# Optimization experiments

Hardware: AMD Instinct MI355X
Metric: run time of the kernel (lower is better)

Reference implementation:

```python
import jax, jax.numpy as jnp
import numpy as np

B, T, H = 128, 1024, 512


def setup_inputs() -> dict:
    key = jax.random.key(0)
    ks = jax.random.split(key, 14)
    s = 1.0 / np.sqrt(H)
    u = lambda k, shape: jax.random.uniform(k, shape, jnp.float32, -s, s)
    return {
        "x": jax.random.normal(ks[0], (B, T, 1), jnp.float32),
        "mask": jax.random.randint(ks[1], (B, T, 1), 0, 2).astype(bool),
        # forward GRU (PyTorch layout: weight_ih [3H,1], weight_hh [3H,H], gate order r,z,n)
        "wf_ih": u(ks[2], (3 * H, 1)),
        "wf_hh": u(ks[3], (3 * H, H)),
        "bf_ih": u(ks[4], (3 * H,)),
        "bf_hh": u(ks[5], (3 * H,)),
        # backward GRU
        "wb_ih": u(ks[6], (3 * H, 1)),
        "wb_hh": u(ks[7], (3 * H, H)),
        "bb_ih": u(ks[8], (3 * H,)),
        "bb_hh": u(ks[9], (3 * H,)),
        # predictor: Linear(H,H) -> ReLU -> Linear(H,1) -> Tanh
        "p_w1": u(ks[10], (H, H)),
        "p_b1": u(ks[11], (H,)),
        "p_w2": u(ks[12], (1, H)),
        "p_b2": u(ks[13], (1,)),
    }


def _gru_cell(h, x_in, w_ih, w_hh, b_ih, b_hh):
    # h: [B,H], x_in: [B,1]; PyTorch GRU gate order (r, z, n)
    gi = x_in @ w_ih.T + b_ih  # [B,3H]
    gh = h @ w_hh.T + b_hh     # [B,3H]
    i_r, i_z, i_n = jnp.split(gi, 3, axis=-1)
    h_r, h_z, h_n = jnp.split(gh, 3, axis=-1)
    r = jax.nn.sigmoid(i_r + h_r)
    z = jax.nn.sigmoid(i_z + h_z)
    n = jnp.tanh(i_n + r * h_n)
    return (1.0 - z) * n + z * h


def reference(x, mask, wf_ih, wf_hh, bf_ih, bf_hh, wb_ih, wb_hh, bb_ih, bb_hh,
              p_w1, p_b1, p_w2, p_b2):
    bsz = x.shape[0]
    hid = wf_hh.shape[1]

    def predictor(h):  # [B,H] -> [B,1]
        return jnp.tanh(jax.nn.relu(h @ p_w1.T + p_b1) @ p_w2.T + p_b2)

    xs_f = jnp.swapaxes(x, 0, 1)      # [T,B,1]
    ms_f = jnp.swapaxes(mask, 0, 1)   # [T,B,1]
    xs_b = xs_f[::-1]
    ms_b = ms_f[::-1]

    def step(carry, inp):
        h_f, h_b = carry
        xf, mf, xb, mb = inp
        # masked positions replaced by predictor output (x*~m + pred*m)
        xf_in = jnp.where(mf, predictor(h_f), xf)
        xb_in = jnp.where(mb, predictor(h_b), xb)
        h_f = _gru_cell(h_f, xf_in, wf_ih, wf_hh, bf_ih, bf_hh)
        h_b = _gru_cell(h_b, xb_in, wb_ih, wb_hh, bb_ih, bb_hh)
        return (h_f, h_b), (h_f, h_b)

    h0 = jnp.zeros((bsz, hid), x.dtype)
    _, (hf_seq, hb_seq) = jax.lax.scan(step, (h0, h0), (xs_f, ms_f, xs_b, ms_b))
    # forward stack in time order; backward stack reversed back to time order
    h_stack = jnp.concatenate([hf_seq, hb_seq[::-1]], axis=-1)  # [T,B,2H]
    return jnp.swapaxes(h_stack, 0, 1)  # [B,T,2H]
```

## Files before the change

kernel.cpp:

```cpp
#include <hip/hip_runtime.h>
#include <hip/hip_bf16.h>


#define T_STEPS 1024
#define H_DIM   512
#define NBLK    256

__device__ __forceinline__ float bf2f(unsigned int u){
  union { unsigned int i; float f; } v; v.i = u << 16; return v.f;
}
__device__ __forceinline__ float ldw(const float* p){ return *p; }
__device__ __forceinline__ float ldw(const __hip_bfloat16* p){
  unsigned short s = *(const unsigned short*)p; return bf2f((unsigned int)s);
}
__device__ __forceinline__ void stw(float* p, float v){ *p = v; }
__device__ __forceinline__ void stw(__hip_bfloat16* p, float v){ *p = __float2bfloat16(v); }

__global__ void probe_kernel(const unsigned int* __restrict__ mw,
                             const unsigned int* __restrict__ ww,
                             int* __restrict__ codes){
  __shared__ unsigned int fl[5];
  if(threadIdx.x < 5) fl[threadIdx.x] = 0u;
  __syncthreads();
  unsigned int l0=0,l1=0,l2=0,l3=0,l4=0;
  for(int i=threadIdx.x; i<32768; i+=256){
    const unsigned int w = mw[i];
    #pragma unroll
    for(int bb=0;bb<4;bb++){
      const unsigned int by = (w >> (8*bb)) & 0xFFu;
      if(by > 1u) l0 = 1u;
      if(bb!=0 && by==1u) l1 = 1u;
    }
    const unsigned int hlo = w & 0xFFFFu, hhi = w >> 16;
    if(!(hlo==0u || hlo==0x3F80u) || !(hhi==0u || hhi==0x3F80u)) l2 = 1u;
    if(hlo == 0x3F80u) l3 = 1u;
  }
  for(int i=threadIdx.x; i<768; i+=256){
    const unsigned int w = ww[i];
    const unsigned int hlo = w & 0xFFFFu;
    if(hlo != 0u && ((hlo>>7)&0xFFu) >= 128u) l4 = 1u;
  }
  if(l0) atomicOr(&fl[0],1u);
  if(l1) atomicOr(&fl[1],1u);
  if(l2) atomicOr(&fl[2],1u);
  if(l3) atomicOr(&fl[3],1u);
  if(l4) atomicOr(&fl[4],1u);
  __syncthreads();
  if(threadIdx.x==0){
    int mcode;
    if(!fl[0] && fl[1])      mcode = 1;
    else if(!fl[2] && fl[3]) mcode = 2;
    else                     mcode = 4;
    codes[0] = mcode;
    codes[1] = fl[4] ? 1 : 0;
    codes[2] = 0;
    codes[3] = 0;
  }
}

__device__ __forceinline__ void grid_bar(int* cnt, int& nbar){
  __syncthreads();
  if(threadIdx.x==0){
    __threadfence();
    __hip_atomic_fetch_add(cnt, 1, __ATOMIC_RELAXED, __HIP_MEMORY_SCOPE_AGENT);
    nbar += NBLK;
    while(__hip_atomic_load(cnt, __ATOMIC_RELAXED, __HIP_MEMORY_SCOPE_AGENT) < nbar)
      __builtin_amdgcn_s_sleep(1);
    __threadfence();
  }
  __syncthreads();
}

template<typename WT, typename OT>
__device__ void body(const void* xv, const void* mkv,
                     const void* wfih, const void* wfhh, const void* bfih, const void* bfhh,
                     const void* wbih, const void* wbhh, const void* bbih, const void* bbhh,
                     const void* pw1v, const void* pb1v, const void* pw2v, const void* pb2v,
                     int mcode, OT* __restrict__ out, float* H_T, float* S, int* cnt,
                     float* wsl, float* wih, float* bih, float* bhh,
                     float* pb1c, float* pw2c, float* red, float* xsh)
{
  const int w   = (int)blockIdx.x;
  const int tid = (int)threadIdx.x;
  const int dir = w >> 7;
  const int b   = w & 127;
  const int colbase = (w & 127) * 16;

  const WT* x  = (const WT*)xv;
  const unsigned char* mk = (const unsigned char*)mkv;

  const WT* whhA  = (const WT*)(dir ? wbhh : wfhh);
  const WT* wrows = (colbase < 1536)
                  ? (whhA + (size_t)colbase * H_DIM)
                  : ((const WT*)pw1v + (size_t)(colbase - 1536) * H_DIM);
  for(int idx = tid; idx < 16*512; idx += 256){
    const int r = idx >> 9, k = idx & 511;
    wsl[r*516 + k] = ldw(wrows + (size_t)r*512 + k);
  }
  const WT* wihp = (const WT*)(dir ? wbih : wfih);
  const WT* bihp = (const WT*)(dir ? bbih : bfih);
  const WT* bhhp = (const WT*)(dir ? bbhh : bfhh);
  for(int i=tid;i<1536;i+=256){ wih[i]=ldw(wihp+i); bih[i]=ldw(bihp+i); bhh[i]=ldw(bhhp+i); }
  for(int i=tid;i<512;i+=256){ pb1c[i]=ldw((const WT*)pb1v+i); pw2c[i]=ldw((const WT*)pw2v+i); }
  const float pb2s = ldw((const WT*)pb2v);

  H_T[w*512 + tid]       = 0.f;
  H_T[w*512 + 256 + tid] = 0.f;

  int nbar = 0;
  grid_bar(cnt, nbar);

  const int   cA  = tid >> 5;
  const int   bg  = tid & 31;
  const int   b0  = bg * 4;
  const float* HbA = H_T + dir*65536;
  const float* wr0 = wsl + cA*516;
  const float* wr1 = wsl + (cA+8)*516;
  float*      SbA = S + (size_t)dir*128*2048 + colbase;

  const int j1 = tid, j2 = tid + 256;
  const float* Sb2 = S + ((size_t)dir*128 + b)*2048;

  float hp1 = 0.f, hp2 = 0.f;

  for(int t=0; t<T_STEPS; t++){
    float aA0=0.f,aA1=0.f,aA2=0.f,aA3=0.f;
    float aB0=0.f,aB1=0.f,aB2=0.f,aB3=0.f;
    for(int k=0;k<512;k+=4){
      const float4 w0 = *(const float4*)(wr0 + k);
      const float4 w1 = *(const float4*)(wr1 + k);
      const float* hp = HbA + k*128 + b0;
      const float4 h0 = *(const float4*)(hp);
      const float4 h1 = *(const float4*)(hp + 128);
      const float4 h2 = *(const float4*)(hp + 256);
      const float4 h3 = *(const float4*)(hp + 384);
      aA0=fmaf(w0.x,h0.x,aA0); aA1=fmaf(w0.x,h0.y,aA1); aA2=fmaf(w0.x,h0.z,aA2); aA3=fmaf(w0.x,h0.w,aA3);
      aB0=fmaf(w1.x,h0.x,aB0); aB1=fmaf(w1.x,h0.y,aB1); aB2=fmaf(w1.x,h0.z,aB2); aB3=fmaf(w1.x,h0.w,aB3);
      aA0=fmaf(w0.y,h1.x,aA0); aA1=fmaf(w0.y,h1.y,aA1); aA2=fmaf(w0.y,h1.z,aA2); aA3=fmaf(w0.y,h1.w,aA3);
      aB0=fmaf(w1.y,h1.x,aB0); aB1=fmaf(w1.y,h1.y,aB1); aB2=fmaf(w1.y,h1.z,aB2); aB3=fmaf(w1.y,h1.w,aB3);
      aA0=fmaf(w0.z,h2.x,aA0); aA1=fmaf(w0.z,h2.y,aA1); aA2=fmaf(w0.z,h2.z,aA2); aA3=fmaf(w0.z,h2.w,aA3);
      aB0=fmaf(w1.z,h2.x,aB0); aB1=fmaf(w1.z,h2.y,aB1); aB2=fmaf(w1.z,h2.z,aB2); aB3=fmaf(w1.z,h2.w,aB3);
      aA0=fmaf(w0.w,h3.x,aA0); aA1=fmaf(w0.w,h3.y,aA1); aA2=fmaf(w0.w,h3.z,aA2); aA3=fmaf(w0.w,h3.w,aA3);
      aB0=fmaf(w1.w,h3.x,aB0); aB1=fmaf(w1.w,h3.y,aB1); aB2=fmaf(w1.w,h3.z,aB2); aB3=fmaf(w1.w,h3.w,aB3);
    }
    {
      float* sp = SbA + (size_t)b0*2048 + cA;
      sp[0]      = aA0;  sp[8]      = aB0;
      sp[2048]   = aA1;  sp[2048+8] = aB1;
      sp[4096]   = aA2;  sp[4096+8] = aB2;
      sp[6144]   = aA3;  sp[6144+8] = aB3;
    }
    grid_bar(cnt, nbar);

    const int ts = dir ? (T_STEPS-1-t) : t;
    const float s_r1 = Sb2[j1],      s_r2 = Sb2[j2];
    const float s_z1 = Sb2[512+j1],  s_z2 = Sb2[512+j2];
    const float s_n1 = Sb2[1024+j1], s_n2 = Sb2[1024+j2];
    const float sp1  = Sb2[1536+j1], sp2  = Sb2[1536+j2];

    {
      float u1 = sp1 + pb1c[j1]; u1 = u1 > 0.f ? u1 : 0.f;
      float u2 = sp2 + pb1c[j2]; u2 = u2 > 0.f ? u2 : 0.f;
      float v = fmaf(u1, pw2c[j1], u2*pw2c[j2]);
      #pragma unroll
      for(int off=32; off; off>>=1) v += __shfl_xor(v, off, 64);
      if((tid & 63)==0) red[tid>>6] = v;
    }
    __syncthreads();
    if(tid==0){
      const size_t idx = (size_t)b*T_STEPS + ts;
      bool mfl;
      if(mcode==1)      mfl = mk[idx] != 0;
      else if(mcode==2) mfl = ((const unsigned short*)mk)[idx] != 0;
      else              mfl = ((const unsigned int*)mk)[idx]  != 0;
      const float xraw = ldw(x + idx);
      const float xp = tanhf(red[0]+red[1]+red[2]+red[3] + pb2s);
      xsh[0] = mfl ? xp : xraw;
    }
    __syncthreads();
    const float xin = xsh[0];

    const float gr1 = s_r1 + bhh[j1];
    const float gz1 = s_z1 + bhh[512+j1];
    const float gn1 = s_n1 + bhh[1024+j1];
    const float ir1 = fmaf(xin, wih[j1],       bih[j1]);
    const float iz1 = fmaf(xin, wih[512+j1],   bih[512+j1]);
    const float in1 = fmaf(xin, wih[1024+j1],  bih[1024+j1]);
    const float r1  = 1.f/(1.f+__expf(-(ir1+gr1)));
    const float z1  = 1.f/(1.f+__expf(-(iz1+gz1)));
    const float n1  = tanhf(fmaf(r1, gn1, in1));
    const float hn1 = (1.f-z1)*n1 + z1*hp1;

    const float gr2 = s_r2 + bhh[j2];
    const float gz2 = s_z2 + bhh[512+j2];
    const float gn2 = s_n2 + bhh[1024+j2];
    const float ir2 = fmaf(xin, wih[j2],       bih[j2]);
    const float iz2 = fmaf(xin, wih[512+j2],   bih[512+j2]);
    const float in2 = fmaf(xin, wih[1024+j2],  bih[1024+j2]);
    const float r2  = 1.f/(1.f+__expf(-(ir2+gr2)));
    const float z2  = 1.f/(1.f+__expf(-(iz2+gz2)));
    const float n2  = tanhf(fmaf(r2, gn2, in2));
    const float hn2 = (1.f-z2)*n2 + z2*hp2;

    hp1 = hn1; hp2 = hn2;

    {
      OT* op = out + ((size_t)b*T_STEPS + ts)*(2*H_DIM) + (size_t)dir*H_DIM;
      stw(op + j1, hn1); stw(op + j2, hn2);
      float* Ht = H_T + dir*65536;
      Ht[j1*128 + b] = hn1;
      Ht[j2*128 + b] = hn2;
    }
    grid_bar(cnt, nbar);
  }
}

__global__ __launch_bounds__(256, 1)
void rnn_kernel(const void* i0,const void* i1,const void* i2,const void* i3,
                const void* i4,const void* i5,const void* i6,const void* i7,
                const void* i8,const void* i9,const void* i10,const void* i11,
                const void* i12,const void* i13, int* codes, void* out, float* ws)
{
  __shared__ float wsl[16*516];
  __shared__ float wih[1536], bih[1536], bhh[1536];
  __shared__ float pb1c[512], pw2c[512];
  __shared__ float red[4];
  __shared__ float xsh[1];

  float* H_T = ws;
  float* S   = ws + 2*512*128;
  int*   cnt = codes + 2;

  if(codes[1]==0)
    body<__hip_bfloat16,__hip_bfloat16>(i0,i1,i2,i3,i4,i5,i6,i7,i8,i9,i10,i11,i12,i13,
        codes[0], (__hip_bfloat16*)out, H_T, S, cnt,
        wsl, wih, bih, bhh, pb1c, pw2c, red, xsh);
  else
    body<float,float>(i0,i1,i2,i3,i4,i5,i6,i7,i8,i9,i10,i11,i12,i13,
        codes[0], (float*)out, H_T, S, cnt,
        wsl, wih, bih, bhh, pb1c, pw2c, red, xsh);
}

extern "C" void kernel_launch(void* const* d_in, const int* in_sizes, int n_in,
                              void* d_out, int out_size, void* d_ws, size_t ws_size,
                              hipStream_t stream)
{
  (void)in_sizes; (void)n_in; (void)out_size; (void)ws_size;
  int*   codes = (int*)d_ws;
  float* ws    = (float*)((char*)d_ws + 512);
  probe_kernel<<<1, 256, 0, stream>>>((const unsigned int*)d_in[1],
                                      (const unsigned int*)d_in[2], codes);
  rnn_kernel<<<NBLK, 256, 0, stream>>>(d_in[0],d_in[1],d_in[2],d_in[3],d_in[4],
                                       d_in[5],d_in[6],d_in[7],d_in[8],d_in[9],
                                       d_in[10],d_in[11],d_in[12],d_in[13],
                                       codes, d_out, ws);
}
```

Before: 83.62 ms.

## Use hierarchical grid barrier with per-group flags and row-major hidden state

Replaces the single-counter grid barrier with a two-level barrier: 16 padded group counters feed a top counter, and the last arriver writes per-group release flags that blocks spin on. Release/acquire fences replace full threadfences. The hidden state buffer moves from transposed to row-major per batch, so the matvec reads contiguous float4 rows per batch element and the state write-back is coalesced. Per-gate weights and biases are moved from shared memory into registers. This targets contention on one atomic counter across 256 blocks at every step, at the cost of extra atomics on the critical path and higher register pressure.

```diff
diff --git a/kernel.cpp b/kernel.cpp
--- a/kernel.cpp
+++ b/kernel.cpp
@@ -45,6 +45,7 @@
   if(l2) atomicOr(&fl[2],1u);
   if(l3) atomicOr(&fl[3],1u);
   if(l4) atomicOr(&fl[4],1u);
+  for(int i=threadIdx.x; i<1792; i+=256) codes[256+i] = 0;
   __syncthreads();
   if(threadIdx.x==0){
     int mcode;
@@ -53,20 +54,30 @@
     else                     mcode = 4;
     codes[0] = mcode;
     codes[1] = fl[4] ? 1 : 0;
-    codes[2] = 0;
-    codes[3] = 0;
-  }
-}
-
-__device__ __forceinline__ void grid_bar(int* cnt, int& nbar){
+  }
+}
+
+__device__ __forceinline__ void grid_barrier(int* bar, int ep, int grp){
   __syncthreads();
   if(threadIdx.x==0){
-    __threadfence();
-    __hip_atomic_fetch_add(cnt, 1, __ATOMIC_RELAXED, __HIP_MEMORY_SCOPE_AGENT);
-    nbar += NBLK;
-    while(__hip_atomic_load(cnt, __ATOMIC_RELAXED, __HIP_MEMORY_SCOPE_AGENT) < nbar)
-      __builtin_amdgcn_s_sleep(1);
-    __threadfence();
+    __builtin_amdgcn_fence(__ATOMIC_RELEASE, "agent");
+    const int old = __hip_atomic_fetch_add(bar + grp*32, 1,
+                      __ATOMIC_RELAXED, __HIP_MEMORY_SCOPE_AGENT);
+    if(old == ep*16 - 1){
+      const int r2 = __hip_atomic_fetch_add(bar + 16*32, 1,
+                      __ATOMIC_RELAXED, __HIP_MEMORY_SCOPE_AGENT);
+      if(r2 == ep*16 - 1){
+        #pragma unroll
+        for(int g=0; g<16; ++g)
+          __hip_atomic_store(bar + (18+g)*32, ep,
+                             __ATOMIC_RELAXED, __HIP_MEMORY_SCOPE_AGENT);
+      }
+    }
+    int* myflag = bar + (18+grp)*32;
+    while(__hip_atomic_load(myflag, __ATOMIC_RELAXED,
+                            __HIP_MEMORY_SCOPE_AGENT) < ep)
+      __builtin_amdgcn_s_sleep(4);
+    __builtin_amdgcn_fence(__ATOMIC_ACQUIRE, "agent");
   }
   __syncthreads();
 }
@@ -76,14 +87,14 @@
                      const void* wfih, const void* wfhh, const void* bfih, const void* bfhh,
                      const void* wbih, const void* wbhh, const void* bbih, const void* bbhh,
                      const void* pw1v, const void* pb1v, const void* pw2v, const void* pb2v,
-                     int mcode, OT* __restrict__ out, float* H_T, float* S, int* cnt,
-                     float* wsl, float* wih, float* bih, float* bhh,
-                     float* pb1c, float* pw2c, float* red, float* xsh)
+                     int mcode, OT* __restrict__ out, float* H_B, float* S, int* bar,
+                     float* wsl, float* red, float* xsh)
 {
   const int w   = (int)blockIdx.x;
   const int tid = (int)threadIdx.x;
   const int dir = w >> 7;
   const int b   = w & 127;
+  const int grp = w & 15;
   const int colbase = (w & 127) * 16;
 
   const WT* x  = (const WT*)xv;
@@ -97,28 +108,42 @@
     const int r = idx >> 9, k = idx & 511;
     wsl[r*516 + k] = ldw(wrows + (size_t)r*512 + k);
   }
+
   const WT* wihp = (const WT*)(dir ? wbih : wfih);
   const WT* bihp = (const WT*)(dir ? bbih : bfih);
   const WT* bhhp = (const WT*)(dir ? bbhh : bfhh);
-  for(int i=tid;i<1536;i+=256){ wih[i]=ldw(wihp+i); bih[i]=ldw(bihp+i); bhh[i]=ldw(bhhp+i); }
-  for(int i=tid;i<512;i+=256){ pb1c[i]=ldw((const WT*)pb1v+i); pw2c[i]=ldw((const WT*)pw2v+i); }
-  const float pb2s = ldw((const WT*)pb2v);
-
-  H_T[w*512 + tid]       = 0.f;
-  H_T[w*512 + 256 + tid] = 0.f;
-
-  int nbar = 0;
-  grid_bar(cnt, nbar);
+  const int j1 = tid, j2 = tid + 256;
+  const float wi_r1=ldw(wihp+j1),      wi_r2=ldw(wihp+j2);
+  const float wi_z1=ldw(wihp+512+j1),  wi_z2=ldw(wihp+512+j2);
+  const float wi_n1=ldw(wihp+1024+j1), wi_n2=ldw(wihp+1024+j2);
+  const float bi_r1=ldw(bihp+j1),      bi_r2=ldw(bihp+j2);
+  const float bi_z1=ldw(bihp+512+j1),  bi_z2=ldw(bihp+512+j2);
+  const float bi_n1=ldw(bihp+1024+j1), bi_n2=ldw(bihp+1024+j2);
+  const float bh_r1=ldw(bhhp+j1),      bh_r2=ldw(bhhp+j2);
+  const float bh_z1=ldw(bhhp+512+j1),  bh_z2=ldw(bhhp+512+j2);
+  const float bh_n1=ldw(bhhp+1024+j1), bh_n2=ldw(bhhp+1024+j2);
+  const float pb11=ldw((const WT*)pb1v+j1), pb12=ldw((const WT*)pb1v+j2);
+  const float pw21=ldw((const WT*)pw2v+j1), pw22=ldw((const WT*)pw2v+j2);
+  const float pb2s=ldw((const WT*)pb2v);
+
+  {
+    float* hrow = H_B + ((size_t)dir*128 + b)*512;
+    hrow[tid] = 0.f; hrow[tid+256] = 0.f;
+  }
+  int ep = 0;
+  grid_barrier(bar, ++ep, grp);
 
   const int   cA  = tid >> 5;
   const int   bg  = tid & 31;
   const int   b0  = bg * 4;
-  const float* HbA = H_T + dir*65536;
   const float* wr0 = wsl + cA*516;
   const float* wr1 = wsl + (cA+8)*516;
+  const float* HbA = H_B + (size_t)dir*128*512;
+  const float* h0p = HbA + (size_t)(b0+0)*512;
+  const float* h1p = HbA + (size_t)(b0+1)*512;
+  const float* h2p = HbA + (size_t)(b0+2)*512;
+  const float* h3p = HbA + (size_t)(b0+3)*512;
   float*      SbA = S + (size_t)dir*128*2048 + colbase;
-
-  const int j1 = tid, j2 = tid + 256;
   const float* Sb2 = S + ((size_t)dir*128 + b)*2048;
 
   float hp1 = 0.f, hp2 = 0.f;
@@ -129,19 +154,18 @@
     for(int k=0;k<512;k+=4){
       const float4 w0 = *(const float4*)(wr0 + k);
       const float4 w1 = *(const float4*)(wr1 + k);
-      const float* hp = HbA + k*128 + b0;
-      const float4 h0 = *(const float4*)(hp);
-      const float4 h1 = *(const float4*)(hp + 128);
-      const float4 h2 = *(const float4*)(hp + 256);
-      const float4 h3 = *(const float4*)(hp + 384);
-      aA0=fmaf(w0.x,h0.x,aA0); aA1=fmaf(w0.x,h0.y,aA1); aA2=fmaf(w0.x,h0.z,aA2); aA3=fmaf(w0.x,h0.w,aA3);
-      aB0=fmaf(w1.x,h0.x,aB0); aB1=fmaf(w1.x,h0.y,aB1); aB2=fmaf(w1.x,h0.z,aB2); aB3=fmaf(w1.x,h0.w,aB3);
-      aA0=fmaf(w0.y,h1.x,aA0); aA1=fmaf(w0.y,h1.y,aA1); aA2=fmaf(w0.y,h1.z,aA2); aA3=fmaf(w0.y,h1.w,aA3);
-      aB0=fmaf(w1.y,h1.x,aB0); aB1=fmaf(w1.y,h1.y,aB1); aB2=fmaf(w1.y,h1.z,aB2); aB3=fmaf(w1.y,h1.w,aB3);
-      aA0=fmaf(w0.z,h2.x,aA0); aA1=fmaf(w0.z,h2.y,aA1); aA2=fmaf(w0.z,h2.z,aA2); aA3=fmaf(w0.z,h2.w,aA3);
-      aB0=fmaf(w1.z,h2.x,aB0); aB1=fmaf(w1.z,h2.y,aB1); aB2=fmaf(w1.z,h2.z,aB2); aB3=fmaf(w1.z,h2.w,aB3);
-      aA0=fmaf(w0.w,h3.x,aA0); aA1=fmaf(w0.w,h3.y,aA1); aA2=fmaf(w0.w,h3.z,aA2); aA3=fmaf(w0.w,h3.w,aA3);
-      aB0=fmaf(w1.w,h3.x,aB0); aB1=fmaf(w1.w,h3.y,aB1); aB2=fmaf(w1.w,h3.z,aB2); aB3=fmaf(w1.w,h3.w,aB3);
+      const float4 h0 = *(const float4*)(h0p + k);
+      const float4 h1 = *(const float4*)(h1p + k);
+      const float4 h2 = *(const float4*)(h2p + k);
+      const float4 h3 = *(const float4*)(h3p + k);
+      aA0=fmaf(w0.x,h0.x,aA0); aA0=fmaf(w0.y,h0.y,aA0); aA0=fmaf(w0.z,h0.z,aA0); aA0=fmaf(w0.w,h0.w,aA0);
+      aA1=fmaf(w0.x,h1.x,aA1); aA1=fmaf(w0.y,h1.y,aA1); aA1=fmaf(w0.z,h1.z,aA1); aA1=fmaf(w0.w,h1.w,aA1);
+      aA2=fmaf(w0.x,h2.x,aA2); aA2=fmaf(w0.y,h2.y,aA2); aA2=fmaf(w0.z,h2.z,aA2); aA2=fmaf(w0.w,h2.w,aA2);
+      aA3=fmaf(w0.x,h3.x,aA3); aA3=fmaf(w0.y,h3.y,aA3); aA3=fmaf(w0.z,h3.z,aA3); aA3=fmaf(w0.w,h3.w,aA3);
+      aB0=fmaf(w1.x,h0.x,aB0); aB0=fmaf(w1.y,h0.y,aB0); aB0=fmaf(w1.z,h0.z,aB0); aB0=fmaf(w1.w,h0.w,aB0);
+      aB1=fmaf(w1.x,h1.x,aB1); aB1=fmaf(w1.y,h1.y,aB1); aB1=fmaf(w1.z,h1.z,aB1); aB1=fmaf(w1.w,h1.w,aB1);
+      aB2=fmaf(w1.x,h2.x,aB2); aB2=fmaf(w1.y,h2.y,aB2); aB2=fmaf(w1.z,h2.z,aB2); aB2=fmaf(w1.w,h2.w,aB2);
+      aB3=fmaf(w1.x,h3.x,aB3); aB3=fmaf(w1.y,h3.y,aB3); aB3=fmaf(w1.z,h3.z,aB3); aB3=fmaf(w1.w,h3.w,aB3);
     }
     {
       float* sp = SbA + (size_t)b0*2048 + cA;
@@ -150,7 +174,7 @@
       sp[4096]   = aA2;  sp[4096+8] = aB2;
       sp[6144]   = aA3;  sp[6144+8] = aB3;
     }
-    grid_bar(cnt, nbar);
+    grid_barrier(bar, ++ep, grp);
 
     const int ts = dir ? (T_STEPS-1-t) : t;
     const float s_r1 = Sb2[j1],      s_r2 = Sb2[j2];
@@ -159,9 +183,9 @@
     const float sp1  = Sb2[1536+j1], sp2  = Sb2[1536+j2];
 
     {
-      float u1 = sp1 + pb1c[j1]; u1 = u1 > 0.f ? u1 : 0.f;
-      float u2 = sp2 + pb1c[j2]; u2 = u2 > 0.f ? u2 : 0.f;
-      float v = fmaf(u1, pw2c[j1], u2*pw2c[j2]);
+      float u1 = sp1 + pb11; u1 = u1 > 0.f ? u1 : 0.f;
+      float u2 = sp2 + pb12; u2 = u2 > 0.f ? u2 : 0.f;
+      float v = fmaf(u1, pw21, u2*pw22);
       #pragma unroll
       for(int off=32; off; off>>=1) v += __shfl_xor(v, off, 64);
       if((tid & 63)==0) red[tid>>6] = v;
@@ -180,26 +204,14 @@
     __syncthreads();
     const float xin = xsh[0];
 
-    const float gr1 = s_r1 + bhh[j1];
-    const float gz1 = s_z1 + bhh[512+j1];
-    const float gn1 = s_n1 + bhh[1024+j1];
-    const float ir1 = fmaf(xin, wih[j1],       bih[j1]);
-    const float iz1 = fmaf(xin, wih[512+j1],   bih[512+j1]);
-    const float in1 = fmaf(xin, wih[1024+j1],  bih[1024+j1]);
-    const float r1  = 1.f/(1.f+__expf(-(ir1+gr1)));
-    const float z1  = 1.f/(1.f+__expf(-(iz1+gz1)));
-    const float n1  = tanhf(fmaf(r1, gn1, in1));
+    const float r1  = 1.f/(1.f+__expf(-(fmaf(xin, wi_r1, bi_r1) + s_r1 + bh_r1)));
+    const float z1  = 1.f/(1.f+__expf(-(fmaf(xin, wi_z1, bi_z1) + s_z1 + bh_z1)));
+    const float n1  = tanhf(fmaf(r1, s_n1 + bh_n1, fmaf(xin, wi_n1, bi_n1)));
     const float hn1 = (1.f-z1)*n1 + z1*hp1;
 
-    const float gr2 = s_r2 + bhh[j2];
-    const float gz2 = s_z2 + bhh[512+j2];
-    const float gn2 = s_n2 + bhh[1024+j2];
-    const float ir2 = fmaf(xin, wih[j2],       bih[j2]);
-    const float iz2 = fmaf(xin, wih[512+j2],   bih[512+j2]);
-    const float in2 = fmaf(xin, wih[1024+j2],  bih[1024+j2]);
-    const float r2  = 1.f/(1.f+__expf(-(ir2+gr2)));
-    const float z2  = 1.f/(1.f+__expf(-(iz2+gz2)));
-    const float n2  = tanhf(fmaf(r2, gn2, in2));
+    const float r2  = 1.f/(1.f+__expf(-(fmaf(xin, wi_r2, bi_r2) + s_r2 + bh_r2)));
+    const float z2  = 1.f/(1.f+__expf(-(fmaf(xin, wi_z2, bi_z2) + s_z2 + bh_z2)));
+    const float n2  = tanhf(fmaf(r2, s_n2 + bh_n2, fmaf(xin, wi_n2, bi_n2)));
     const float hn2 = (1.f-z2)*n2 + z2*hp2;
 
     hp1 = hn1; hp2 = hn2;
@@ -207,11 +219,10 @@
     {
       OT* op = out + ((size_t)b*T_STEPS + ts)*(2*H_DIM) + (size_t)dir*H_DIM;
       stw(op + j1, hn1); stw(op + j2, hn2);
-      float* Ht = H_T + dir*65536;
-      Ht[j1*128 + b] = hn1;
-      Ht[j2*128 + b] = hn2;
-    }
-    grid_bar(cnt, nbar);
+      float* hrow = H_B + ((size_t)dir*128 + b)*512;
+      hrow[j1] = hn1; hrow[j2] = hn2;
+    }
+    grid_barrier(bar, ++ep, grp);
   }
 }
 
@@ -222,23 +233,19 @@
                 const void* i12,const void* i13, int* codes, void* out, float* ws)
 {
   __shared__ float wsl[16*516];
-  __shared__ float wih[1536], bih[1536], bhh[1536];
-  __shared__ float pb1c[512], pw2c[512];
   __shared__ float red[4];
   __shared__ float xsh[1];
 
-  float* H_T = ws;
-  float* S   = ws + 2*512*128;
-  int*   cnt = codes + 2;
+  float* H_B = ws;
+  float* S   = ws + 2*128*512;
+  int*   bar = codes + 256;
 
   if(codes[1]==0)
     body<__hip_bfloat16,__hip_bfloat16>(i0,i1,i2,i3,i4,i5,i6,i7,i8,i9,i10,i11,i12,i13,
-        codes[0], (__hip_bfloat16*)out, H_T, S, cnt,
-        wsl, wih, bih, bhh, pb1c, pw2c, red, xsh);
+        codes[0], (__hip_bfloat16*)out, H_B, S, bar, wsl, red, xsh);
   else
     body<float,float>(i0,i1,i2,i3,i4,i5,i6,i7,i8,i9,i10,i11,i12,i13,
-        codes[0], (float*)out, H_T, S, cnt,
-        wsl, wih, bih, bhh, pb1c, pw2c, red, xsh);
+        codes[0], (float*)out, H_B, S, bar, wsl, red, xsh);
 }
 
 extern "C" void kernel_launch(void* const* d_in, const int* in_sizes, int n_in,
@@ -247,7 +254,7 @@
 {
   (void)in_sizes; (void)n_in; (void)out_size; (void)ws_size;
   int*   codes = (int*)d_ws;
-  float* ws    = (float*)((char*)d_ws + 512);
+  float* ws    = (float*)((char*)d_ws + 8192);
   probe_kernel<<<1, 256, 0, stream>>>((const unsigned int*)d_in[1],
                                       (const unsigned int*)d_in[2], codes);
   rnn_kernel<<<NBLK, 256, 0, stream>>>(d_in[0],d_in[1],d_in[2],d_in[3],d_in[4],
```

Result: no change. 82.53 ms (-1.3%).
